# Performance work log

Hardware: AMD Instinct MI355X
Metric: run time of the kernel (lower is better)

## Reference

```python
import jax, jax.numpy as jnp
import numpy as np

N_HEAD = 16


def setup_inputs() -> dict:
    key = jax.random.key(0)
    ks = jax.random.split(key, 7)
    B, T, C = 2, 2048, 1024
    s = 1.0 / np.sqrt(C)
    return {
        "x": jax.random.normal(ks[0], (B, T, C), jnp.float32),
        "Wq": jax.random.normal(ks[1], (C, C), jnp.float32) * s,
        "bq": jnp.zeros((C,), jnp.float32),
        "Wk": jax.random.normal(ks[2], (C, C), jnp.float32) * s,
        "bk": jnp.zeros((C,), jnp.float32),
        "Wv": jax.random.normal(ks[3], (C, C), jnp.float32) * s,
        "bv": jnp.zeros((C,), jnp.float32),
    }


def reference(x, Wq, bq, Wk, bk, Wv, bv):
    B, T, C = x.shape
    H = N_HEAD
    D = C // H
    # qkv projections -> [B, H, T, D]
    def proj(W, b):
        return (x @ W.T + b).reshape(B, T, H, D).transpose(0, 2, 1, 3)
    q = proj(Wq, bq)
    k = proj(Wk, bk)
    v = proj(Wv, bv)
    # scaled causal attention with materialized [B,H,T,T] scores
    att = jnp.einsum("bhqd,bhkd->bhqk", q, k) / jnp.sqrt(jnp.asarray(D, x.dtype))
    causal = jnp.tril(jnp.ones((T, T), bool))
    att = jnp.where(causal[None, None], att, -jnp.inf)
    att = jax.nn.softmax(att, axis=-1)
    y = jnp.einsum("bhqk,bhkd->bhqd", att, v)
    y = y.transpose(0, 2, 1, 3).reshape(B, T, C)
    return (y, k, v)  # matches torch return (y, new_kv_cache=(k, v))
```

## Files before the change

### kernel.cpp

```cpp
#include <hip/hip_runtime.h>
#include <hip/hip_bf16.h>
#include <stdint.h>

typedef __attribute__((ext_vector_type(8))) short bf16x8;
typedef __attribute__((ext_vector_type(4))) float f32x4;

#define DEVINL __device__ __forceinline__

DEVINL unsigned short f2bf(float f) {
  unsigned int u = __builtin_bit_cast(unsigned int, f);
  u += 0x7fffu + ((u >> 16) & 1u);
  return (unsigned short)(u >> 16);
}

DEVINL void gload_lds16(const void* gptr, void* lptr) {
  __builtin_amdgcn_global_load_lds(
      (__attribute__((address_space(1))) void*)(uintptr_t)gptr,
      (__attribute__((address_space(3))) void*)(uint32_t)(uintptr_t)lptr,
      16, 0, 0);
}

__global__ __launch_bounds__(256) void cvt_bf16_kernel(const float* __restrict__ src,
                                                       unsigned short* __restrict__ dst,
                                                       int n) {
  int i = (blockIdx.x * 256 + threadIdx.x) * 4;
  if (i >= n) return;
  const float4 v = *reinterpret_cast<const float4*>(src + i);
  ushort4 o;
  o.x = f2bf(v.x); o.y = f2bf(v.y); o.z = f2bf(v.z); o.w = f2bf(v.w);
  *reinterpret_cast<ushort4*>(dst + i) = o;
}

__global__ __launch_bounds__(256) void qkv_gemm_kernel(
    const unsigned short* __restrict__ xbf,
    const unsigned short* __restrict__ wcat,
    const float* __restrict__ bq,
    const float* __restrict__ bk,
    const float* __restrict__ bv,
    float* __restrict__ out_k,
    float* __restrict__ out_v,
    unsigned short* __restrict__ qbf,
    unsigned short* __restrict__ kbf,
    unsigned short* __restrict__ vtr)
{
  __shared__ unsigned short As[128 * 32];
  __shared__ unsigned short Bs[128 * 32];
  const int t = threadIdx.x;
  const int l = t & 63;
  const int w = t >> 6;
  const int lr = l & 15, lg = l >> 4;
  const int wr = w >> 1, wc = w & 1;
  const int m0 = blockIdx.y * 128;
  const int n0 = blockIdx.x * 128;

  const int row0 = (t * 8) >> 5, col0 = (t * 8) & 31;
  const int row1 = ((256 + t) * 8) >> 5, col1 = ((256 + t) * 8) & 31;
  const unsigned short* aG0 = xbf + (m0 + row0) * 1024 + col0;
  const unsigned short* aG1 = xbf + (m0 + row1) * 1024 + col1;
  const unsigned short* bG0 = wcat + (n0 + row0) * 1024 + col0;
  const unsigned short* bG1 = wcat + (n0 + row1) * 1024 + col1;
  unsigned short* aL0 = As + t * 8;
  unsigned short* aL1 = As + (256 + t) * 8;
  unsigned short* bL0 = Bs + t * 8;
  unsigned short* bL1 = Bs + (256 + t) * 8;

  const int aOff = (wr * 64 + lr) * 32 + 8 * lg;
  const int bOff = (wc * 64 + lr) * 32 + 8 * lg;

  f32x4 acc[4][4];
  const f32x4 zf = {0.f, 0.f, 0.f, 0.f};
#pragma unroll
  for (int i = 0; i < 4; i++)
#pragma unroll
    for (int j = 0; j < 4; j++) acc[i][j] = zf;

  for (int kt = 0; kt < 1024; kt += 32) {
    gload_lds16(aG0 + kt, aL0);
    gload_lds16(aG1 + kt, aL1);
    gload_lds16(bG0 + kt, bL0);
    gload_lds16(bG1 + kt, bL1);
    __syncthreads();
    bf16x8 af[4], bfr[4];
#pragma unroll
    for (int mi = 0; mi < 4; mi++)
      af[mi] = *reinterpret_cast<const bf16x8*>(As + aOff + mi * 16 * 32);
#pragma unroll
    for (int ni = 0; ni < 4; ni++)
      bfr[ni] = *reinterpret_cast<const bf16x8*>(Bs + bOff + ni * 16 * 32);
#pragma unroll
    for (int mi = 0; mi < 4; mi++)
#pragma unroll
      for (int ni = 0; ni < 4; ni++)
        acc[mi][ni] = __builtin_amdgcn_mfma_f32_16x16x32_bf16(af[mi], bfr[ni], acc[mi][ni], 0, 0, 0);
    __syncthreads();
  }

  const int which = n0 >> 10;
  const float* bias = (which == 0) ? bq : (which == 1) ? bk : bv;
#pragma unroll
  for (int ni = 0; ni < 4; ni++) {
    const int n = n0 + wc * 64 + ni * 16 + lr;
    const int co = n & 1023;
    const float bb = bias[co];
    const int h = co >> 6, d = co & 63;
#pragma unroll
    for (int mi = 0; mi < 4; mi++) {
#pragma unroll
      for (int r = 0; r < 4; r++) {
        const int m = m0 + wr * 64 + mi * 16 + 4 * lg + r;
        const float val = acc[mi][ni][r] + bb;
        const int bb_ = m >> 11, tt = m & 2047;
        const int bh = bb_ * 16 + h;
        const int idx = (bh * 2048 + tt) * 64 + d;
        if (which == 0) {
          qbf[idx] = f2bf(val);
        } else if (which == 1) {
          out_k[idx] = val;
          kbf[idx] = f2bf(val);
        } else {
          out_v[idx] = val;
          vtr[(bh * 64 + d) * 2048 + tt] = f2bf(val);
        }
      }
    }
  }
}

__global__ __launch_bounds__(512) void attn_kernel(
    const unsigned short* __restrict__ qbf,
    const unsigned short* __restrict__ kbf,
    const unsigned short* __restrict__ vtr,
    float* __restrict__ y)
{
  __shared__ unsigned short pbuf[8][16 * 80];
  const int w = threadIdx.x >> 6, l = threadIdx.x & 63;
  const int lr = l & 15, lg = l >> 4;

  const int blk = blockIdx.x;
  const int xcd = blk & 7, slot = blk >> 3;
  const int bh = xcd * 4 + (slot & 3);
  const int p = slot >> 2;
  const int qt = (w < 4) ? p : (31 - p);
  const int qbase = qt * 64 + (w & 3) * 16;
  const int b = bh >> 4, h = bh & 15;

  const unsigned short* Q = qbf + bh * 2048 * 64;
  const unsigned short* K = kbf + bh * 2048 * 64;
  const unsigned short* V = vtr + bh * 64 * 2048;
  unsigned short* pb = pbuf[w];

  const int qrow = qbase + lr;
  const bf16x8 qf0 = *reinterpret_cast<const bf16x8*>(Q + qrow * 64 + 8 * lg);
  const bf16x8 qf1 = *reinterpret_cast<const bf16x8*>(Q + qrow * 64 + 32 + 8 * lg);

  float mi = -1e30f, li = 0.f;
  f32x4 acc[4];
  const f32x4 zf = {0.f, 0.f, 0.f, 0.f};
#pragma unroll
  for (int dt = 0; dt < 4; dt++) acc[dt] = zf;

  const int nkv = qbase + 16;
  for (int kb = 0; kb < nkv; kb += 64) {
    f32x4 s[4];
#pragma unroll
    for (int kt = 0; kt < 4; kt++) {
      const unsigned short* kr = K + (kb + kt * 16 + lr) * 64;
      const bf16x8 kf0 = *reinterpret_cast<const bf16x8*>(kr + 8 * lg);
      const bf16x8 kf1 = *reinterpret_cast<const bf16x8*>(kr + 32 + 8 * lg);
      f32x4 t = zf;
      t = __builtin_amdgcn_mfma_f32_16x16x32_bf16(kf0, qf0, t, 0, 0, 0);
      t = __builtin_amdgcn_mfma_f32_16x16x32_bf16(kf1, qf1, t, 0, 0, 0);
      s[kt] = t;
    }
    float v[16];
#pragma unroll
    for (int kt = 0; kt < 4; kt++)
#pragma unroll
      for (int r = 0; r < 4; r++) {
        const int key = kb + kt * 16 + 4 * lg + r;
        const float val = s[kt][r] * 0.125f;
        v[kt * 4 + r] = (key > qrow) ? -1e30f : val;
      }
    float t8[8];
#pragma unroll
    for (int i = 0; i < 8; i++) t8[i] = fmaxf(v[2 * i], v[2 * i + 1]);
    float t4[4];
#pragma unroll
    for (int i = 0; i < 4; i++) t4[i] = fmaxf(t8[2 * i], t8[2 * i + 1]);
    float mr = fmaxf(fmaxf(t4[0], t4[1]), fmaxf(t4[2], t4[3]));
    mr = fmaxf(mr, __shfl_xor(mr, 16));
    mr = fmaxf(mr, __shfl_xor(mr, 32));
    const float mnew = fmaxf(mi, mr);
    const float alpha = __expf(mi - mnew);
    mi = mnew;
#pragma unroll
    for (int i = 0; i < 16; i++) v[i] = __expf(v[i] - mnew);
    float s8[8];
#pragma unroll
    for (int i = 0; i < 8; i++) s8[i] = v[2 * i] + v[2 * i + 1];
    float s4[4];
#pragma unroll
    for (int i = 0; i < 4; i++) s4[i] = s8[2 * i] + s8[2 * i + 1];
    float sr = (s4[0] + s4[1]) + (s4[2] + s4[3]);
    sr += __shfl_xor(sr, 16);
    sr += __shfl_xor(sr, 32);
    li = li * alpha + sr;
#pragma unroll
    for (int dt = 0; dt < 4; dt++)
#pragma unroll
      for (int r = 0; r < 4; r++) acc[dt][r] *= alpha;
#pragma unroll
    for (int kt = 0; kt < 4; kt++)
#pragma unroll
      for (int i = 0; i < 2; i++) {
        const unsigned int pk =
            ((unsigned int)f2bf(v[kt * 4 + 2 * i + 1]) << 16) | f2bf(v[kt * 4 + 2 * i]);
        *reinterpret_cast<unsigned int*>(pb + lr * 80 + kt * 16 + 4 * lg + 2 * i) = pk;
      }
    const bf16x8 pf0 = *reinterpret_cast<const bf16x8*>(pb + lr * 80 + 8 * lg);
    const bf16x8 pf1 = *reinterpret_cast<const bf16x8*>(pb + lr * 80 + 32 + 8 * lg);
#pragma unroll
    for (int dt = 0; dt < 4; dt++) {
      const unsigned short* vr = V + (dt * 16 + lr) * 2048 + kb;
      const bf16x8 vf0 = *reinterpret_cast<const bf16x8*>(vr + 8 * lg);
      const bf16x8 vf1 = *reinterpret_cast<const bf16x8*>(vr + 32 + 8 * lg);
      acc[dt] = __builtin_amdgcn_mfma_f32_16x16x32_bf16(vf0, pf0, acc[dt], 0, 0, 0);
      acc[dt] = __builtin_amdgcn_mfma_f32_16x16x32_bf16(vf1, pf1, acc[dt], 0, 0, 0);
    }
  }

  const float inv = 1.0f / li;
  float* yb = y + (b * 2048 + qrow) * 1024 + h * 64;
#pragma unroll
  for (int dt = 0; dt < 4; dt++) {
    float4 o;
    o.x = acc[dt][0] * inv; o.y = acc[dt][1] * inv;
    o.z = acc[dt][2] * inv; o.w = acc[dt][3] * inv;
    *reinterpret_cast<float4*>(yb + dt * 16 + 4 * lg) = o;
  }
}

extern "C" void kernel_launch(void* const* d_in, const int* in_sizes, int n_in,
                              void* d_out, int out_size, void* d_ws, size_t ws_size,
                              hipStream_t stream) {
  const float* x  = (const float*)d_in[0];
  const float* Wq = (const float*)d_in[1];
  const float* bq = (const float*)d_in[2];
  const float* Wk = (const float*)d_in[3];
  const float* bk = (const float*)d_in[4];
  const float* Wv = (const float*)d_in[5];
  const float* bv = (const float*)d_in[6];

  float* y = (float*)d_out;
  float* out_k = y + 4194304;
  float* out_v = y + 8388608;

  char* wsb = (char*)d_ws;
  unsigned short* xbf  = (unsigned short*)(wsb);
  unsigned short* wcat = (unsigned short*)(wsb + (8u  << 20));
  unsigned short* qbf  = (unsigned short*)(wsb + (14u << 20));
  unsigned short* kbf  = (unsigned short*)(wsb + (22u << 20));
  unsigned short* vtr  = (unsigned short*)(wsb + (30u << 20));

  cvt_bf16_kernel<<<4096, 256, 0, stream>>>(x, xbf, 4194304);
  cvt_bf16_kernel<<<1024, 256, 0, stream>>>(Wq, wcat, 1048576);
  cvt_bf16_kernel<<<1024, 256, 0, stream>>>(Wk, wcat + 1048576, 1048576);
  cvt_bf16_kernel<<<1024, 256, 0, stream>>>(Wv, wcat + 2097152, 1048576);

  qkv_gemm_kernel<<<dim3(24, 32), 256, 0, stream>>>(xbf, wcat, bq, bk, bv,
                                                    out_k, out_v, qbf, kbf, vtr);

  attn_kernel<<<512, 512, 0, stream>>>(qbf, kbf, vtr, y);
}
```

Before: 259.3 us.

## Widen attention KV tile to 128 with lazy rescale, exp2, and packed bf16 cvt

Doubles the per-iteration key block from 64 to 128 keys, folds log2(e) into the score scale so exp2f replaces __expf, and skips the running-max rescale of the accumulator unless some lane's max grows by more than a threshold. Probabilities are packed with the hardware v_cvt_pk_bf16_f32 instruction instead of manual rounding. This is meant to cut exp cost, rescale work and loop overhead per key, at the cost of more registers, a larger LDS buffer and values that can exceed 1 before normalization.

```diff
diff --git a/kernel.cpp b/kernel.cpp
--- a/kernel.cpp
+++ b/kernel.cpp
@@ -11,6 +11,12 @@
   unsigned int u = __builtin_bit_cast(unsigned int, f);
   u += 0x7fffu + ((u >> 16) & 1u);
   return (unsigned short)(u >> 16);
+}
+
+DEVINL unsigned int cvt_pk_bf16(float lo, float hi) {
+  unsigned int r;
+  asm("v_cvt_pk_bf16_f32 %0, %1, %2" : "=v"(r) : "v"(lo), "v"(hi));
+  return r;
 }
 
 DEVINL void gload_lds16(const void* gptr, void* lptr) {
@@ -132,7 +138,7 @@
     const unsigned short* __restrict__ vtr,
     float* __restrict__ y)
 {
-  __shared__ unsigned short pbuf[8][16 * 80];
+  __shared__ unsigned short pbuf[8][16 * 136];
   const int w = threadIdx.x >> 6, l = threadIdx.x & 63;
   const int lr = l & 15, lg = l >> 4;
 
@@ -153,6 +159,9 @@
   const bf16x8 qf0 = *reinterpret_cast<const bf16x8*>(Q + qrow * 64 + 8 * lg);
   const bf16x8 qf1 = *reinterpret_cast<const bf16x8*>(Q + qrow * 64 + 32 + 8 * lg);
 
+  const float cs = 0.125f * 1.4426950408889634f;
+  const float THR = 8.0f * 1.4426950408889634f;
+
   float mi = -1e30f, li = 0.f;
   f32x4 acc[4];
   const f32x4 zf = {0.f, 0.f, 0.f, 0.f};
@@ -160,10 +169,10 @@
   for (int dt = 0; dt < 4; dt++) acc[dt] = zf;
 
   const int nkv = qbase + 16;
-  for (int kb = 0; kb < nkv; kb += 64) {
-    f32x4 s[4];
-#pragma unroll
-    for (int kt = 0; kt < 4; kt++) {
+  for (int kb = 0; kb < nkv; kb += 128) {
+    f32x4 s[8];
+#pragma unroll
+    for (int kt = 0; kt < 8; kt++) {
       const unsigned short* kr = K + (kb + kt * 16 + lr) * 64;
       const bf16x8 kf0 = *reinterpret_cast<const bf16x8*>(kr + 8 * lg);
       const bf16x8 kf1 = *reinterpret_cast<const bf16x8*>(kr + 32 + 8 * lg);
@@ -172,60 +181,68 @@
       t = __builtin_amdgcn_mfma_f32_16x16x32_bf16(kf1, qf1, t, 0, 0, 0);
       s[kt] = t;
     }
-    float v[16];
-#pragma unroll
-    for (int kt = 0; kt < 4; kt++)
+    float v[32];
+#pragma unroll
+    for (int kt = 0; kt < 8; kt++)
 #pragma unroll
       for (int r = 0; r < 4; r++) {
         const int key = kb + kt * 16 + 4 * lg + r;
-        const float val = s[kt][r] * 0.125f;
+        const float val = s[kt][r] * cs;
         v[kt * 4 + r] = (key > qrow) ? -1e30f : val;
       }
+    float t16[16];
+#pragma unroll
+    for (int i = 0; i < 16; i++) t16[i] = fmaxf(v[2 * i], v[2 * i + 1]);
     float t8[8];
 #pragma unroll
-    for (int i = 0; i < 8; i++) t8[i] = fmaxf(v[2 * i], v[2 * i + 1]);
+    for (int i = 0; i < 8; i++) t8[i] = fmaxf(t16[2 * i], t16[2 * i + 1]);
     float t4[4];
 #pragma unroll
     for (int i = 0; i < 4; i++) t4[i] = fmaxf(t8[2 * i], t8[2 * i + 1]);
     float mr = fmaxf(fmaxf(t4[0], t4[1]), fmaxf(t4[2], t4[3]));
     mr = fmaxf(mr, __shfl_xor(mr, 16));
     mr = fmaxf(mr, __shfl_xor(mr, 32));
-    const float mnew = fmaxf(mi, mr);
-    const float alpha = __expf(mi - mnew);
-    mi = mnew;
-#pragma unroll
-    for (int i = 0; i < 16; i++) v[i] = __expf(v[i] - mnew);
-    float s8[8];
-#pragma unroll
-    for (int i = 0; i < 8; i++) s8[i] = v[2 * i] + v[2 * i + 1];
-    float s4[4];
-#pragma unroll
-    for (int i = 0; i < 4; i++) s4[i] = s8[2 * i] + s8[2 * i + 1];
-    float sr = (s4[0] + s4[1]) + (s4[2] + s4[3]);
+    if (__any(mr > mi + THR)) {
+      const float mnew = fmaxf(mi, mr);
+      const float alpha = exp2f(mi - mnew);
+      mi = mnew;
+      li *= alpha;
+#pragma unroll
+      for (int dt = 0; dt < 4; dt++)
+#pragma unroll
+        for (int r = 0; r < 4; r++) acc[dt][r] *= alpha;
+    }
+#pragma unroll
+    for (int i = 0; i < 32; i++) v[i] = exp2f(v[i] - mi);
+    float u16[16];
+#pragma unroll
+    for (int i = 0; i < 16; i++) u16[i] = v[2 * i] + v[2 * i + 1];
+    float u8[8];
+#pragma unroll
+    for (int i = 0; i < 8; i++) u8[i] = u16[2 * i] + u16[2 * i + 1];
+    float u4[4];
+#pragma unroll
+    for (int i = 0; i < 4; i++) u4[i] = u8[2 * i] + u8[2 * i + 1];
+    float sr = (u4[0] + u4[1]) + (u4[2] + u4[3]);
     sr += __shfl_xor(sr, 16);
     sr += __shfl_xor(sr, 32);
-    li = li * alpha + sr;
-#pragma unroll
-    for (int dt = 0; dt < 4; dt++)
-#pragma unroll
-      for (int r = 0; r < 4; r++) acc[dt][r] *= alpha;
-#pragma unroll
-    for (int kt = 0; kt < 4; kt++)
+    li += sr;
+#pragma unroll
+    for (int kt = 0; kt < 8; kt++)
 #pragma unroll
       for (int i = 0; i < 2; i++) {
-        const unsigned int pk =
-            ((unsigned int)f2bf(v[kt * 4 + 2 * i + 1]) << 16) | f2bf(v[kt * 4 + 2 * i]);
-        *reinterpret_cast<unsigned int*>(pb + lr * 80 + kt * 16 + 4 * lg + 2 * i) = pk;
-      }
-    const bf16x8 pf0 = *reinterpret_cast<const bf16x8*>(pb + lr * 80 + 8 * lg);
-    const bf16x8 pf1 = *reinterpret_cast<const bf16x8*>(pb + lr * 80 + 32 + 8 * lg);
-#pragma unroll
-    for (int dt = 0; dt < 4; dt++) {
-      const unsigned short* vr = V + (dt * 16 + lr) * 2048 + kb;
-      const bf16x8 vf0 = *reinterpret_cast<const bf16x8*>(vr + 8 * lg);
-      const bf16x8 vf1 = *reinterpret_cast<const bf16x8*>(vr + 32 + 8 * lg);
-      acc[dt] = __builtin_amdgcn_mfma_f32_16x16x32_bf16(vf0, pf0, acc[dt], 0, 0, 0);
-      acc[dt] = __builtin_amdgcn_mfma_f32_16x16x32_bf16(vf1, pf1, acc[dt], 0, 0, 0);
+        const unsigned int pk = cvt_pk_bf16(v[kt * 4 + 2 * i], v[kt * 4 + 2 * i + 1]);
+        *reinterpret_cast<unsigned int*>(pb + lr * 136 + kt * 16 + 4 * lg + 2 * i) = pk;
+      }
+#pragma unroll
+    for (int kc = 0; kc < 4; kc++) {
+      const bf16x8 pf = *reinterpret_cast<const bf16x8*>(pb + lr * 136 + kc * 32 + 8 * lg);
+#pragma unroll
+      for (int dt = 0; dt < 4; dt++) {
+        const bf16x8 vf = *reinterpret_cast<const bf16x8*>(
+            V + (dt * 16 + lr) * 2048 + kb + kc * 32 + 8 * lg);
+        acc[dt] = __builtin_amdgcn_mfma_f32_16x16x32_bf16(vf, pf, acc[dt], 0, 0, 0);
+      }
     }
   }
 
```

Result: no change. 259.6 us (+0.1%).
